# Kernel tuning notes

Hardware: AMD Instinct MI355X
Metric: run time of the kernel (lower is better)

The kernel has to match this reference:

```python
import jax, jax.numpy as jnp
import numpy as np

B, N, C = 16, 4096, 512
FR = 2          # fr_ratio
NH = 8          # num_heads
CF = C // FR    # 256, q/k/v projection dim
HD = (C // NH) // FR  # 32, per-head dim after fr reduction
EPS = 1e-4


def _abs_clamp(t):
    # sign(t) * clamp(|t|, 1e-4, 1e4), as in the torch module's abs_clamp
    return jnp.sign(t) * jnp.clip(jnp.abs(t), 1e-4, 1e4)


def setup_inputs() -> dict:
    key = jax.random.key(0)
    ks = jax.random.split(key, 8)
    s = 0.02  # trunc_normal_(std=0.02) init scale
    return {
        "query": jax.random.normal(ks[0], (B, N, C), jnp.float32),
        "Wq": jax.random.normal(ks[1], (CF, C), jnp.float32) * s,
        "bq": jnp.zeros((CF,), jnp.float32),
        "Wk": jax.random.normal(ks[2], (CF, C), jnp.float32) * s,
        "bk": jnp.zeros((CF,), jnp.float32),
        "Wv": jax.random.normal(ks[3], (CF, C), jnp.float32) * s,
        "bv": jnp.zeros((CF,), jnp.float32),
        "Wo": jax.random.normal(ks[4], (C, CF), jnp.float32) * s,
        "bo": jnp.zeros((C,), jnp.float32),
        "Wse1": jax.random.normal(ks[5], (C // 2, C), jnp.float32) * s,
        "Wse2": jax.random.normal(ks[6], (C, C // 2), jnp.float32) * s,
        "H": 64,
        "W": 64,
    }


def reference(query, Wq, bq, Wk, bk, Wv, bv, Wo, bo, Wse1, Wse2, H, W):
    Bq, Nq, Cq = query.shape  # N == H*W
    # --- squeeze-excitation gate: mean over tokens -> 2-layer MLP -> sigmoid
    se = jnp.mean(query, axis=1)                                   # [B, C]
    se = jax.nn.sigmoid(jax.nn.relu(se @ Wse1.T) @ Wse2.T)         # [B, C]

    # --- q/k/v projections (sr_ratio=1: k/v from full-length query)
    q = jax.nn.relu(query @ Wq.T + bq).reshape(Bq, Nq, NH, HD)     # [B,N,h,d]
    k = jax.nn.relu(query @ Wk.T + bk).reshape(Bq, Nq, NH, HD)
    v = (query @ Wv.T + bv).reshape(Bq, Nq, NH, HD)

    # --- cosFormer-style 2D positional feature maps
    c = jnp.pi / 2
    idx = jnp.arange(Nq)
    a = (c * (idx // W).astype(query.dtype) / H)[None, :, None, None]  # row angle
    b = (c * (idx % W).astype(query.dtype) / W)[None, :, None, None]   # col angle
    q_ = jnp.concatenate([q * jnp.cos(a), q * jnp.sin(a),
                          q * jnp.cos(b), q * jnp.sin(b)], axis=-1)    # [B,N,h,4d]
    k_ = jnp.concatenate([k * jnp.cos(a), k * jnp.sin(a),
                          k * jnp.cos(b), k * jnp.sin(b)], axis=-1)    # sr_ratio=1 -> same angles

    # --- linear attention: kv state then q lookup, with abs-clamping
    kv = _abs_clamp(jnp.einsum('bnhf,bnhd->bhfd', k_, v))          # [B,h,4d,d]
    k_sum = jnp.sum(k_, axis=1, keepdims=True)                     # [B,1,h,4d]
    z = _abs_clamp(1.0 / (jnp.sum(q_ * k_sum, axis=-1) + EPS))     # [B,N,h]
    out = _abs_clamp(jnp.einsum('bnhf,bhfd->bnhd', q_, kv))        # [B,N,h,d]
    out = _abs_clamp(out * z[..., None])

    # --- output projection + SE residual gating
    out = _abs_clamp(out.reshape(Bq, Nq, CF) @ Wo.T + bo)          # [B,N,C]
    out = _abs_clamp(out + out * se[:, None, :])
    return out
```

## Files before the change

### kernel.cpp

```cpp
#include <hip/hip_runtime.h>
#include <math.h>

#define B_   16
#define N_   4096
#define C_   512
#define CF_  256
#define NH_  8
#define HD_  32
#define FHD_ 128
#define BN_  (B_ * N_)
#define EPS_ 1e-4f
#define PI2F 1.5707963267948966f

typedef _Float16 half8 __attribute__((ext_vector_type(8)));
typedef _Float16 half4 __attribute__((ext_vector_type(4)));
typedef float f32x4 __attribute__((ext_vector_type(4)));
typedef unsigned short u16x8 __attribute__((ext_vector_type(8)));

__device__ __forceinline__ float abs_clamp(float t) {
    float a = fminf(fmaxf(fabsf(t), 1e-4f), 1e4f);
    return t > 0.f ? a : (t < 0.f ? -a : 0.f);
}
__device__ __forceinline__ void gld16(const void* g, void* l) {
    __builtin_amdgcn_global_load_lds(
        (const __attribute__((address_space(1))) void*)g,
        (__attribute__((address_space(3))) void*)l, 16, 0, 0);
}

__global__ __launch_bounds__(256) void se_sum_kernel(const float* __restrict__ q,
                                                     float* __restrict__ sesum,
                                                     _Float16* __restrict__ q16) {
    int b = blockIdx.x, chunk = blockIdx.y;
    int t = threadIdx.x;
    int c = (t & 127) * 4;
    int tok0 = chunk * 64 + (t >> 7) * 32;
    const float* p = q + ((size_t)b * N_ + tok0) * C_ + c;
    _Float16* o = q16 + ((size_t)b * N_ + tok0) * C_ + c;
    float a0 = 0.f, a1 = 0.f, a2 = 0.f, a3 = 0.f;
#pragma unroll 4
    for (int n = 0; n < 32; n++) {
        float4 v = *(const float4*)(p + (size_t)n * C_);
        a0 += v.x; a1 += v.y; a2 += v.z; a3 += v.w;
        half4 hv;
        hv[0] = (_Float16)v.x; hv[1] = (_Float16)v.y;
        hv[2] = (_Float16)v.z; hv[3] = (_Float16)v.w;
        *(half4*)(o + (size_t)n * C_) = hv;
    }
    atomicAdd(&sesum[b * C_ + c + 0], a0);
    atomicAdd(&sesum[b * C_ + c + 1], a1);
    atomicAdd(&sesum[b * C_ + c + 2], a2);
    atomicAdd(&sesum[b * C_ + c + 3], a3);
}

__global__ __launch_bounds__(256) void se_gate_kernel(const float* __restrict__ sesum,
                                                      const float* __restrict__ Wse1,
                                                      const float* __restrict__ Wse2,
                                                      float* __restrict__ segate) {
    __shared__ float sm[C_];
    __shared__ float hm[C_ / 2];
    int b = blockIdx.x, t = threadIdx.x;
    sm[t]       = sesum[b * C_ + t]       * (1.f / N_);
    sm[t + 256] = sesum[b * C_ + t + 256] * (1.f / N_);
    __syncthreads();
    {
        const float* w = Wse1 + (size_t)t * C_;
        float acc = 0.f;
        for (int c2 = 0; c2 < C_; c2++) acc += sm[c2] * w[c2];
        hm[t] = fmaxf(acc, 0.f);
    }
    __syncthreads();
    for (int r = 0; r < 2; r++) {
        int c2 = t + r * 256;
        const float* w2 = Wse2 + (size_t)c2 * (C_ / 2);
        float a2 = 0.f;
        for (int j = 0; j < C_ / 2; j++) a2 += hm[j] * w2[j];
        segate[b * C_ + c2] = 1.f / (1.f + expf(-a2));
    }
}

__global__ __launch_bounds__(256) void convert_w(const float* __restrict__ Wq,
                                                 const float* __restrict__ Wk,
                                                 const float* __restrict__ Wv,
                                                 const float* __restrict__ Wo,
                                                 _Float16* __restrict__ wcat,
                                                 _Float16* __restrict__ wo16) {
    int i = blockIdx.x * 256 + threadIdx.x;
    if (i < 768 * 512) {
        int r = i >> 9, c = i & 511;
        float w = (r < 256) ? Wq[(size_t)r * 512 + c]
                : (r < 512) ? Wk[(size_t)(r - 256) * 512 + c]
                            : Wv[(size_t)(r - 512) * 512 + c];
        wcat[i] = (_Float16)w;
    } else {
        int j = i - 768 * 512;
        wo16[j] = (_Float16)Wo[j];
    }
}

__global__ __launch_bounds__(256) void gemm_qkv(
    const _Float16* __restrict__ A16, const _Float16* __restrict__ Bw,
    const float* __restrict__ bq, const float* __restrict__ bk, const float* __restrict__ bv,
    _Float16* __restrict__ Oq, _Float16* __restrict__ kT, _Float16* __restrict__ vT) {
    constexpr int K = 512;
    constexpr int NITER = K / 32;

    __shared__ __align__(16) unsigned short As[2][128 * 32];
    __shared__ __align__(16) unsigned short Bs[2][128 * 32];

    const int t = threadIdx.x;
    const int did = blockIdx.x + 6 * blockIdx.y;
    const int lid = (did & 7) * 384 + (did >> 3);
    const int bx = lid % 6;
    const int Mb = (lid / 6) * 128;
    const int nrow0 = bx * 128;

    const int lane = t & 63;
    const int wv = t >> 6;
    const int mq = (wv >> 1) * 64;
    const int nq = (wv & 1) * 64;
    const int mrow = lane & 15;
    const int kq = lane >> 4;
    const int fragoff = mrow * 32 + ((kq ^ ((mrow >> 1) & 3)) * 8);

    const unsigned char *asrc0, *asrc1, *bsrc0, *bsrc1;
    int off0, off1;
    {
        int cid0 = t, cid1 = t + 256;
        int m0 = cid0 >> 2, c0 = (cid0 & 3) ^ ((m0 >> 1) & 3);
        int m1 = cid1 >> 2, c1 = (cid1 & 3) ^ ((m1 >> 1) & 3);
        asrc0 = (const unsigned char*)(A16 + (size_t)(Mb + m0) * K + c0 * 8);
        asrc1 = (const unsigned char*)(A16 + (size_t)(Mb + m1) * K + c1 * 8);
        bsrc0 = (const unsigned char*)(Bw + (size_t)(nrow0 + m0) * K + c0 * 8);
        bsrc1 = (const unsigned char*)(Bw + (size_t)(nrow0 + m1) * K + c1 * 8);
        off0 = cid0 * 8;
        off1 = cid1 * 8;
    }

    f32x4 acc[4][4];
#pragma unroll
    for (int mi = 0; mi < 4; mi++)
#pragma unroll
        for (int ni = 0; ni < 4; ni++) acc[mi][ni] = (f32x4){0.f, 0.f, 0.f, 0.f};

    gld16(asrc0, &As[0][off0]);
    gld16(asrc1, &As[0][off1]);
    gld16(bsrc0, &Bs[0][off0]);
    gld16(bsrc1, &Bs[0][off1]);
    __syncthreads();

    int cur = 0;
#pragma unroll 1
    for (int it = 0; it < NITER; ++it) {
        if (it + 1 < NITER) {
            gld16(asrc0 + (it + 1) * 64, &As[cur ^ 1][off0]);
            gld16(asrc1 + (it + 1) * 64, &As[cur ^ 1][off1]);
            gld16(bsrc0 + (it + 1) * 64, &Bs[cur ^ 1][off0]);
            gld16(bsrc1 + (it + 1) * 64, &Bs[cur ^ 1][off1]);
        }

        half8 ah[4], bh[4];
#pragma unroll
        for (int mi = 0; mi < 4; mi++)
            ah[mi] = *(const half8*)&As[cur][(mq + mi * 16) * 32 + fragoff];
#pragma unroll
        for (int ni = 0; ni < 4; ni++)
            bh[ni] = *(const half8*)&Bs[cur][(nq + ni * 16) * 32 + fragoff];
#pragma unroll
        for (int mi = 0; mi < 4; mi++)
#pragma unroll
            for (int ni = 0; ni < 4; ni++)
                acc[mi][ni] = __builtin_amdgcn_mfma_f32_16x16x32_f16(ah[mi], bh[ni], acc[mi][ni], 0, 0, 0);

        if (it + 1 < NITER) __syncthreads();
        cur ^= 1;
    }

#pragma unroll
    for (int ni = 0; ni < 4; ni++) {
        int gc = nrow0 + nq + ni * 16 + mrow;
        int mat = gc >> 8;
        int col = gc & 255;
        float bb = (mat == 0 ? bq : mat == 1 ? bk : bv)[col];
        if (mat == 0) {
#pragma unroll
            for (int mi = 0; mi < 4; mi++)
#pragma unroll
                for (int r = 0; r < 4; r++) {
                    int m = Mb + mq + mi * 16 + kq * 4 + r;
                    float v2 = fmaxf(acc[mi][ni][r] + bb, 0.f);
                    Oq[(size_t)m * CF_ + col] = (_Float16)v2;
                }
        } else {
            _Float16* OT = (mat == 1) ? kT : vT;
#pragma unroll
            for (int mi = 0; mi < 4; mi++) {
                int m0r = Mb + mq + mi * 16 + kq * 4;
                half4 hv;
#pragma unroll
                for (int r = 0; r < 4; r++) {
                    float v2 = acc[mi][ni][r] + bb;
                    if (mat == 1) v2 = fmaxf(v2, 0.f);
                    hv[r] = (_Float16)v2;
                }
                *(half4*)&OT[(size_t)col * BN_ + m0r] = hv;
            }
        }
    }
}

__global__ __launch_bounds__(256) void gemm_out(
    const _Float16* __restrict__ A16, const _Float16* __restrict__ Bw,
    const float* __restrict__ bo, const float* __restrict__ sg,
    float* __restrict__ Of) {
    constexpr int K = 256;
    constexpr int NITER = K / 32;

    __shared__ __align__(16) unsigned short As[2][128 * 32];
    __shared__ __align__(16) unsigned short Bs[2][128 * 32];

    const int t = threadIdx.x;
    const int did = blockIdx.x + 4 * blockIdx.y;
    const int lid = (did & 7) * 256 + (did >> 3);
    const int bx = lid & 3;
    const int Mb = (lid >> 2) * 128;
    const int nrow0 = bx * 128;

    const int lane = t & 63;
    const int wv = t >> 6;
    const int mq = (wv >> 1) * 64;
    const int nq = (wv & 1) * 64;
    const int mrow = lane & 15;
    const int kq = lane >> 4;
    const int fragoff = mrow * 32 + ((kq ^ ((mrow >> 1) & 3)) * 8);

    const unsigned char *asrc0, *asrc1, *bsrc0, *bsrc1;
    int off0, off1;
    {
        int cid0 = t, cid1 = t + 256;
        int m0 = cid0 >> 2, c0 = (cid0 & 3) ^ ((m0 >> 1) & 3);
        int m1 = cid1 >> 2, c1 = (cid1 & 3) ^ ((m1 >> 1) & 3);
        asrc0 = (const unsigned char*)(A16 + (size_t)(Mb + m0) * K + c0 * 8);
        asrc1 = (const unsigned char*)(A16 + (size_t)(Mb + m1) * K + c1 * 8);
        bsrc0 = (const unsigned char*)(Bw + (size_t)(nrow0 + m0) * K + c0 * 8);
        bsrc1 = (const unsigned char*)(Bw + (size_t)(nrow0 + m1) * K + c1 * 8);
        off0 = cid0 * 8;
        off1 = cid1 * 8;
    }

    f32x4 acc[4][4];
#pragma unroll
    for (int mi = 0; mi < 4; mi++)
#pragma unroll
        for (int ni = 0; ni < 4; ni++) acc[mi][ni] = (f32x4){0.f, 0.f, 0.f, 0.f};

    gld16(asrc0, &As[0][off0]);
    gld16(asrc1, &As[0][off1]);
    gld16(bsrc0, &Bs[0][off0]);
    gld16(bsrc1, &Bs[0][off1]);
    __syncthreads();

    int cur = 0;
#pragma unroll 1
    for (int it = 0; it < NITER; ++it) {
        if (it + 1 < NITER) {
            gld16(asrc0 + (it + 1) * 64, &As[cur ^ 1][off0]);
            gld16(asrc1 + (it + 1) * 64, &As[cur ^ 1][off1]);
            gld16(bsrc0 + (it + 1) * 64, &Bs[cur ^ 1][off0]);
            gld16(bsrc1 + (it + 1) * 64, &Bs[cur ^ 1][off1]);
        }

        half8 ah[4], bh[4];
#pragma unroll
        for (int mi = 0; mi < 4; mi++)
            ah[mi] = *(const half8*)&As[cur][(mq + mi * 16) * 32 + fragoff];
#pragma unroll
        for (int ni = 0; ni < 4; ni++)
            bh[ni] = *(const half8*)&Bs[cur][(nq + ni * 16) * 32 + fragoff];
#pragma unroll
        for (int mi = 0; mi < 4; mi++)
#pragma unroll
            for (int ni = 0; ni < 4; ni++)
                acc[mi][ni] = __builtin_amdgcn_mfma_f32_16x16x32_f16(ah[mi], bh[ni], acc[mi][ni], 0, 0, 0);

        if (it + 1 < NITER) __syncthreads();
        cur ^= 1;
    }

    int b = Mb >> 12;
#pragma unroll
    for (int ni = 0; ni < 4; ni++) {
        int gc = nrow0 + nq + ni * 16 + mrow;
        float bb = bo[gc];
        float gv = sg[b * C_ + gc];
#pragma unroll
        for (int mi = 0; mi < 4; mi++)
#pragma unroll
            for (int r = 0; r < 4; r++) {
                int m = Mb + mq + mi * 16 + kq * 4 + r;
                float v2 = abs_clamp(acc[mi][ni][r] + bb);
                v2 = abs_clamp(v2 * (1.f + gv));
                Of[(size_t)m * C_ + gc] = v2;
            }
    }
}

__global__ __launch_bounds__(256) void kv_mfma_kernel(const _Float16* __restrict__ kin,
                                                      const _Float16* __restrict__ vin,
                                                      float* __restrict__ kvout,
                                                      float* __restrict__ ksum) {
    __shared__ __align__(16) unsigned short Ah[128 * 128];
    __shared__ __align__(16) unsigned short Bh[48 * 128];

    const int t = threadIdx.x;
    const int c8 = blockIdx.x;
    const int h = blockIdx.y, b = blockIdx.z;
    const int dp = t & 31;
    const int oct = t >> 5;

    {
        int r = 32 + (t >> 4);
        int c = t & 15;
        unsigned short fill = (r == 32) ? (unsigned short)0x3C00 : (unsigned short)0;
        u16x8 z = {fill, fill, fill, fill, fill, fill, fill, fill};
        *(u16x8*)&Bh[r * 128 + ((c ^ (r & 7)) * 8)] = z;
    }

    float cbv[8], sbv[8];
#pragma unroll
    for (int i = 0; i < 8; i++) {
        float ang = (PI2F / 64.f) * (float)(oct * 8 + i);
        cbv[i] = cosf(ang);
        sbv[i] = sinf(ang);
    }

    const int lane = t & 63;
    const int wv = t >> 6;
    const int mrow = lane & 15;
    const int kq = lane >> 4;

    f32x4 acc[2][3];
#pragma unroll
    for (int mi = 0; mi < 2; mi++)
#pragma unroll
        for (int ni = 0; ni < 3; ni++) acc[mi][ni] = (f32x4){0.f, 0.f, 0.f, 0.f};

    int offAa[4], offAb[4];
#pragma unroll
    for (int tvar = 0; tvar < 4; tvar++) {
        int f = tvar * 32 + dp;
        offAa[tvar] = f * 128 + ((oct ^ (f & 7)) * 8);
        offAb[tvar] = f * 128 + (((oct + 8) ^ (f & 7)) * 8);
    }
    const int offBa = dp * 128 + ((oct ^ (dp & 7)) * 8);
    const int offBb = dp * 128 + (((oct + 8) ^ (dp & 7)) * 8);

    const size_t colbase = (size_t)(h * HD_ + dp) * BN_ + (size_t)b * N_;

#pragma unroll 1
    for (int ch = 0; ch < 4; ch++) {
        const int n0 = c8 * 512 + ch * 128;
        const int rr = n0 >> 6;
        float ca0 = cosf((PI2F / 64.f) * (float)rr),       sa0 = sinf((PI2F / 64.f) * (float)rr);
        float ca1 = cosf((PI2F / 64.f) * (float)(rr + 1)), sa1 = sinf((PI2F / 64.f) * (float)(rr + 1));

        const _Float16* kp = kin + colbase + n0 + oct * 8;
        const _Float16* vp = vin + colbase + n0 + oct * 8;
        half8 k8a = *(const half8*)kp;
        half8 k8b = *(const half8*)(kp + 64);
        half8 v8a = *(const half8*)vp;
        half8 v8b = *(const half8*)(vp + 64);
        float ka[8], kb[8];
#pragma unroll
        for (int i = 0; i < 8; i++) { ka[i] = (float)k8a[i]; kb[i] = (float)k8b[i]; }

        __syncthreads();

#pragma unroll
        for (int tvar = 0; tvar < 4; tvar++) {
            half8 ha, hb;
#pragma unroll
            for (int i = 0; i < 8; i++) {
                float fa = (tvar == 0) ? ca0 : (tvar == 1) ? sa0 : (tvar == 2) ? cbv[i] : sbv[i];
                float fb = (tvar == 0) ? ca1 : (tvar == 1) ? sa1 : (tvar == 2) ? cbv[i] : sbv[i];
                ha[i] = (_Float16)(ka[i] * fa);
                hb[i] = (_Float16)(kb[i] * fb);
            }
            *(half8*)&Ah[offAa[tvar]] = ha;
            *(half8*)&Ah[offAb[tvar]] = hb;
        }
        *(half8*)&Bh[offBa] = v8a;
        *(half8*)&Bh[offBb] = v8b;
        __syncthreads();

#pragma unroll
        for (int s = 0; s < 4; s++) {
            int koct = s * 4 + kq;
            half8 ah[2], bh[3];
#pragma unroll
            for (int mi = 0; mi < 2; mi++) {
                int f = (wv * 2 + mi) * 16 + mrow;
                ah[mi] = *(const half8*)&Ah[f * 128 + ((koct ^ (f & 7)) * 8)];
            }
#pragma unroll
            for (int ni = 0; ni < 3; ni++) {
                int nr = ni * 16 + mrow;
                bh[ni] = *(const half8*)&Bh[nr * 128 + ((koct ^ (nr & 7)) * 8)];
            }
#pragma unroll
            for (int mi = 0; mi < 2; mi++)
#pragma unroll
                for (int ni = 0; ni < 3; ni++)
                    acc[mi][ni] = __builtin_amdgcn_mfma_f32_16x16x32_f16(ah[mi], bh[ni], acc[mi][ni], 0, 0, 0);
        }
    }

    float* kvp = kvout + (size_t)(b * NH_ + h) * FHD_ * HD_;
    float* ksp = ksum + (size_t)(b * NH_ + h) * FHD_;
#pragma unroll
    for (int mi = 0; mi < 2; mi++) {
        int mt = wv * 2 + mi;
#pragma unroll
        for (int r = 0; r < 4; r++) {
            int f = mt * 16 + kq * 4 + r;
            atomicAdd(&kvp[(size_t)mrow * FHD_ + f], acc[mi][0][r]);
            atomicAdd(&kvp[(size_t)(16 + mrow) * FHD_ + f], acc[mi][1][r]);
            if (mrow == 0) atomicAdd(&ksp[f], acc[mi][2][r]);
        }
    }
}

__global__ __launch_bounds__(256) void attn_kernel(const _Float16* __restrict__ qbuf,
                                                   const float* __restrict__ kvin,
                                                   const float* __restrict__ ksum,
                                                   _Float16* __restrict__ ob) {
    __shared__ __align__(16) unsigned short Aq[128 * 40];
    __shared__ __align__(16) unsigned short Bk[48 * 128];
    __shared__ __align__(16) float tS[128][4];
    __shared__ float zS[128];

    const int chunk = blockIdx.x;
    const int h = blockIdx.y, b = blockIdx.z;
    const int t = threadIdx.x;
    const int n0 = chunk * 128;

    {
        const float* kvp = kvin + ((size_t)(b * NH_ + h)) * (HD_ * FHD_);
        int d = t >> 3;
        int c0 = (t & 7) * 2;
#pragma unroll
        for (int cc = 0; cc < 2; cc++) {
            int c = c0 + cc;
            const float* src = kvp + (size_t)d * FHD_ + c * 8;
            half8 hv;
#pragma unroll
            for (int i = 0; i < 8; i++) hv[i] = (_Float16)abs_clamp(src[i]);
            *(half8*)&Bk[d * 128 + ((c ^ (d & 7)) * 8)] = hv;
        }
        if (t < 16) {
            const float* ks = ksum + ((size_t)(b * NH_ + h)) * FHD_ + t * 8;
            half8 hv;
#pragma unroll
            for (int i = 0; i < 8; i++) hv[i] = (_Float16)ks[i];
            *(half8*)&Bk[32 * 128 + (t * 8)] = hv;
        } else {
            int idx = t - 16;
            int r = 33 + (idx >> 4), c = idx & 15;
            half8 z = {};
            *(half8*)&Bk[r * 128 + ((c ^ (r & 7)) * 8)] = z;
        }
    }
    {
        int tok = t >> 1, hf = t & 1;
        const _Float16* qp = qbuf + ((size_t)b * N_ + n0 + tok) * CF_ + h * HD_ + hf * 16;
        half8 a0 = *(const half8*)qp;
        half8 a1 = *(const half8*)(qp + 8);
        *(half8*)&Aq[tok * 40 + hf * 16] = a0;
        *(half8*)&Aq[tok * 40 + hf * 16 + 8] = a1;
    }
    if (t < 128) {
        int n = n0 + t;
        float aa = (PI2F / 64.f) * (float)(n >> 6);
        float ab = (PI2F / 64.f) * (float)(n & 63);
        tS[t][0] = cosf(aa); tS[t][1] = sinf(aa);
        tS[t][2] = cosf(ab); tS[t][3] = sinf(ab);
    }
    __syncthreads();

    const int lane = t & 63;
    const int wv = t >> 6;
    const int mrow = lane & 15;
    const int kq = lane >> 4;

    half8 ah[2];
#pragma unroll
    for (int mi = 0; mi < 2; mi++)
        ah[mi] = *(const half8*)&Aq[(wv * 32 + mi * 16 + mrow) * 40 + kq * 8];

    f32x4 acc[4][2][3];
#pragma unroll
    for (int tt = 0; tt < 4; tt++)
#pragma unroll
        for (int mi = 0; mi < 2; mi++)
#pragma unroll
            for (int ni = 0; ni < 3; ni++) acc[tt][mi][ni] = (f32x4){0.f, 0.f, 0.f, 0.f};

#pragma unroll
    for (int tt = 0; tt < 4; tt++) {
        half8 bh[3];
        int cpos = tt * 4 + kq;
#pragma unroll
        for (int ni = 0; ni < 3; ni++) {
            int row = ni * 16 + mrow;
            bh[ni] = *(const half8*)&Bk[row * 128 + ((cpos ^ (row & 7)) * 8)];
        }
#pragma unroll
        for (int mi = 0; mi < 2; mi++)
#pragma unroll
            for (int ni = 0; ni < 3; ni++)
                acc[tt][mi][ni] = __builtin_amdgcn_mfma_f32_16x16x32_f16(ah[mi], bh[ni], acc[tt][mi][ni], 0, 0, 0);
    }

    if (mrow == 0) {
#pragma unroll
        for (int mi = 0; mi < 2; mi++)
#pragma unroll
            for (int r = 0; r < 4; r++) {
                int tok = wv * 32 + mi * 16 + kq * 4 + r;
                float4 tv = *(const float4*)&tS[tok][0];
                float zraw = tv.x * acc[0][mi][2][r] + tv.y * acc[1][mi][2][r]
                           + tv.z * acc[2][mi][2][r] + tv.w * acc[3][mi][2][r];
                zS[tok] = abs_clamp(1.f / (zraw + EPS_));
            }
    }
    __syncthreads();

#pragma unroll
    for (int mi = 0; mi < 2; mi++) {
#pragma unroll
        for (int r = 0; r < 4; r++) {
            int tok = wv * 32 + mi * 16 + kq * 4 + r;
            float4 tv = *(const float4*)&tS[tok][0];
            float z = zS[tok];
            float v0 = tv.x * acc[0][mi][0][r] + tv.y * acc[1][mi][0][r]
                     + tv.z * acc[2][mi][0][r] + tv.w * acc[3][mi][0][r];
            float v1 = tv.x * acc[0][mi][1][r] + tv.y * acc[1][mi][1][r]
                     + tv.z * acc[2][mi][1][r] + tv.w * acc[3][mi][1][r];
            v0 = abs_clamp(abs_clamp(v0) * z);
            v1 = abs_clamp(abs_clamp(v1) * z);
            size_t base = ((size_t)b * N_ + n0 + tok) * CF_ + h * HD_;
            ob[base + mrow] = (_Float16)v0;
            ob[base + 16 + mrow] = (_Float16)v1;
        }
    }
}

extern "C" void kernel_launch(void* const* d_in, const int* in_sizes, int n_in,
                              void* d_out, int out_size, void* d_ws, size_t ws_size,
                              hipStream_t stream) {
    (void)in_sizes; (void)n_in; (void)out_size; (void)ws_size;
    const float* query = (const float*)d_in[0];
    const float* Wq = (const float*)d_in[1];
    const float* bq = (const float*)d_in[2];
    const float* Wk = (const float*)d_in[3];
    const float* bk = (const float*)d_in[4];
    const float* Wv = (const float*)d_in[5];
    const float* bv = (const float*)d_in[6];
    const float* Wo = (const float*)d_in[7];
    const float* bo = (const float*)d_in[8];
    const float* Wse1 = (const float*)d_in[9];
    const float* Wse2 = (const float*)d_in[10];
    float* out = (float*)d_out;

    unsigned char* ws = (unsigned char*)d_ws;
    const size_t MB = 1024ull * 1024ull;
    _Float16* q16 = (_Float16*)(ws + 0);
    _Float16* ob  = (_Float16*)(ws + 0);
    _Float16* qb  = (_Float16*)(ws + 64 * MB);
    _Float16* kbT = (_Float16*)(ws + 96 * MB);
    _Float16* vbT = (_Float16*)(ws + 128 * MB);
    _Float16* wcat = (_Float16*)(ws + 160 * MB);
    _Float16* wo16 = (_Float16*)(ws + 160 * MB + 786432);
    float* kvb = (float*)(ws + 161 * MB);
    float* ksb = (float*)(ws + 163 * MB);
    float* ssb = (float*)(ws + 163 * MB + 65536);
    float* sgb = (float*)(ws + 163 * MB + 98304);

    hipMemsetAsync(kvb, 0, 2097152 + 65536 + 32768, stream);

    convert_w<<<2048, 256, 0, stream>>>(Wq, Wk, Wv, Wo, wcat, wo16);
    se_sum_kernel<<<dim3(B_, 64), 256, 0, stream>>>(query, ssb, q16);
    se_gate_kernel<<<B_, 256, 0, stream>>>(ssb, Wse1, Wse2, sgb);
    gemm_qkv<<<dim3(6, 512), 256, 0, stream>>>(q16, wcat, bq, bk, bv, qb, kbT, vbT);
    kv_mfma_kernel<<<dim3(8, NH_, B_), 256, 0, stream>>>(kbT, vbT, kvb, ksb);
    attn_kernel<<<dim3(32, NH_, B_), 256, 0, stream>>>(qb, kvb, ksb, ob);
    gemm_out<<<dim3(4, 512), 256, 0, stream>>>(ob, wo16, bo, sgb, out);
}
```

Baseline: 515.8 us.

## Triple-buffer GEMM LDS tiles and prefetch all k/v chunks in kv-state kernel

Both fp16 GEMM kernels move from double to triple-buffered LDS tiles. Loads are issued two iterations ahead, with explicit vmcnt waits and a single barrier per iteration in place of two __syncthreads. The kv-state kernel now loads all four k/v chunks into registers up front and fully unrolls the chunk loop, so global load latency overlaps compute. This raises LDS use per block and register pressure, which may reduce occupancy.

```diff
diff --git a/kernel.cpp b/kernel.cpp
--- a/kernel.cpp
+++ b/kernel.cpp
@@ -104,8 +104,8 @@
     constexpr int K = 512;
     constexpr int NITER = K / 32;
 
-    __shared__ __align__(16) unsigned short As[2][128 * 32];
-    __shared__ __align__(16) unsigned short Bs[2][128 * 32];
+    __shared__ __align__(16) unsigned short As[3][128 * 32];
+    __shared__ __align__(16) unsigned short Bs[3][128 * 32];
 
     const int t = threadIdx.x;
     const int did = blockIdx.x + 6 * blockIdx.y;
@@ -146,16 +146,27 @@
     gld16(asrc1, &As[0][off1]);
     gld16(bsrc0, &Bs[0][off0]);
     gld16(bsrc1, &Bs[0][off1]);
-    __syncthreads();
+    gld16(asrc0 + 64, &As[1][off0]);
+    gld16(asrc1 + 64, &As[1][off1]);
+    gld16(bsrc0 + 64, &Bs[1][off0]);
+    gld16(bsrc1 + 64, &Bs[1][off1]);
 
     int cur = 0;
 #pragma unroll 1
     for (int it = 0; it < NITER; ++it) {
         if (it + 1 < NITER) {
-            gld16(asrc0 + (it + 1) * 64, &As[cur ^ 1][off0]);
-            gld16(asrc1 + (it + 1) * 64, &As[cur ^ 1][off1]);
-            gld16(bsrc0 + (it + 1) * 64, &Bs[cur ^ 1][off0]);
-            gld16(bsrc1 + (it + 1) * 64, &Bs[cur ^ 1][off1]);
+            asm volatile("s_waitcnt vmcnt(4)" ::: "memory");
+        } else {
+            asm volatile("s_waitcnt vmcnt(0)" ::: "memory");
+        }
+        __builtin_amdgcn_sched_barrier(0);
+        __builtin_amdgcn_s_barrier();
+        if (it + 2 < NITER) {
+            int nb = cur + 2; if (nb >= 3) nb -= 3;
+            gld16(asrc0 + (it + 2) * 64, &As[nb][off0]);
+            gld16(asrc1 + (it + 2) * 64, &As[nb][off1]);
+            gld16(bsrc0 + (it + 2) * 64, &Bs[nb][off0]);
+            gld16(bsrc1 + (it + 2) * 64, &Bs[nb][off1]);
         }
 
         half8 ah[4], bh[4];
@@ -171,8 +182,7 @@
             for (int ni = 0; ni < 4; ni++)
                 acc[mi][ni] = __builtin_amdgcn_mfma_f32_16x16x32_f16(ah[mi], bh[ni], acc[mi][ni], 0, 0, 0);
 
-        if (it + 1 < NITER) __syncthreads();
-        cur ^= 1;
+        cur = (cur == 2) ? 0 : cur + 1;
     }
 
 #pragma unroll
@@ -215,8 +225,8 @@
     constexpr int K = 256;
     constexpr int NITER = K / 32;
 
-    __shared__ __align__(16) unsigned short As[2][128 * 32];
-    __shared__ __align__(16) unsigned short Bs[2][128 * 32];
+    __shared__ __align__(16) unsigned short As[3][128 * 32];
+    __shared__ __align__(16) unsigned short Bs[3][128 * 32];
 
     const int t = threadIdx.x;
     const int did = blockIdx.x + 4 * blockIdx.y;
@@ -257,16 +267,27 @@
     gld16(asrc1, &As[0][off1]);
     gld16(bsrc0, &Bs[0][off0]);
     gld16(bsrc1, &Bs[0][off1]);
-    __syncthreads();
+    gld16(asrc0 + 64, &As[1][off0]);
+    gld16(asrc1 + 64, &As[1][off1]);
+    gld16(bsrc0 + 64, &Bs[1][off0]);
+    gld16(bsrc1 + 64, &Bs[1][off1]);
 
     int cur = 0;
 #pragma unroll 1
     for (int it = 0; it < NITER; ++it) {
         if (it + 1 < NITER) {
-            gld16(asrc0 + (it + 1) * 64, &As[cur ^ 1][off0]);
-            gld16(asrc1 + (it + 1) * 64, &As[cur ^ 1][off1]);
-            gld16(bsrc0 + (it + 1) * 64, &Bs[cur ^ 1][off0]);
-            gld16(bsrc1 + (it + 1) * 64, &Bs[cur ^ 1][off1]);
+            asm volatile("s_waitcnt vmcnt(4)" ::: "memory");
+        } else {
+            asm volatile("s_waitcnt vmcnt(0)" ::: "memory");
+        }
+        __builtin_amdgcn_sched_barrier(0);
+        __builtin_amdgcn_s_barrier();
+        if (it + 2 < NITER) {
+            int nb = cur + 2; if (nb >= 3) nb -= 3;
+            gld16(asrc0 + (it + 2) * 64, &As[nb][off0]);
+            gld16(asrc1 + (it + 2) * 64, &As[nb][off1]);
+            gld16(bsrc0 + (it + 2) * 64, &Bs[nb][off0]);
+            gld16(bsrc1 + (it + 2) * 64, &Bs[nb][off1]);
         }
 
         half8 ah[4], bh[4];
@@ -282,8 +303,7 @@
             for (int ni = 0; ni < 4; ni++)
                 acc[mi][ni] = __builtin_amdgcn_mfma_f32_16x16x32_f16(ah[mi], bh[ni], acc[mi][ni], 0, 0, 0);
 
-        if (it + 1 < NITER) __syncthreads();
-        cur ^= 1;
+        cur = (cur == 2) ? 0 : cur + 1;
     }
 
     int b = Mb >> 12;
@@ -356,22 +376,29 @@
 
     const size_t colbase = (size_t)(h * HD_ + dp) * BN_ + (size_t)b * N_;
 
-#pragma unroll 1
+    half8 kk[4][2], vv[4][2];
+    {
+        const _Float16* kp0 = kin + colbase + c8 * 512 + oct * 8;
+        const _Float16* vp0 = vin + colbase + c8 * 512 + oct * 8;
+#pragma unroll
+        for (int ch = 0; ch < 4; ch++) {
+            kk[ch][0] = *(const half8*)(kp0 + ch * 128);
+            kk[ch][1] = *(const half8*)(kp0 + ch * 128 + 64);
+            vv[ch][0] = *(const half8*)(vp0 + ch * 128);
+            vv[ch][1] = *(const half8*)(vp0 + ch * 128 + 64);
+        }
+    }
+
+#pragma unroll
     for (int ch = 0; ch < 4; ch++) {
         const int n0 = c8 * 512 + ch * 128;
         const int rr = n0 >> 6;
         float ca0 = cosf((PI2F / 64.f) * (float)rr),       sa0 = sinf((PI2F / 64.f) * (float)rr);
         float ca1 = cosf((PI2F / 64.f) * (float)(rr + 1)), sa1 = sinf((PI2F / 64.f) * (float)(rr + 1));
 
-        const _Float16* kp = kin + colbase + n0 + oct * 8;
-        const _Float16* vp = vin + colbase + n0 + oct * 8;
-        half8 k8a = *(const half8*)kp;
-        half8 k8b = *(const half8*)(kp + 64);
-        half8 v8a = *(const half8*)vp;
-        half8 v8b = *(const half8*)(vp + 64);
         float ka[8], kb[8];
 #pragma unroll
-        for (int i = 0; i < 8; i++) { ka[i] = (float)k8a[i]; kb[i] = (float)k8b[i]; }
+        for (int i = 0; i < 8; i++) { ka[i] = (float)kk[ch][0][i]; kb[i] = (float)kk[ch][1][i]; }
 
         __syncthreads();
 
@@ -388,8 +415,8 @@
             *(half8*)&Ah[offAa[tvar]] = ha;
             *(half8*)&Ah[offAb[tvar]] = hb;
         }
-        *(half8*)&Bh[offBa] = v8a;
-        *(half8*)&Bh[offBb] = v8b;
+        *(half8*)&Bh[offBa] = vv[ch][0];
+        *(half8*)&Bh[offBb] = vv[ch][1];
         __syncthreads();
 
 #pragma unroll
```

New measurement: 525.9 us. About the same (+2.0%).
